# Kernel optimization log

Measured on AMD Instinct MI355X. Metric: run time of the kernel, lower is better.

## Reference

```python
import jax, jax.numpy as jnp
import numpy as np

IN_DIM, HID_DIM, OUT_DIM = 1024, 2048, 1024
DEG1, DEG2 = 8, 8
BATCH = 16384


def cheby_kan_layer(x, coeffs):
    """x: [b, i]; coeffs: [i, o, d+1] -> [b, o].
    Per-feature min-max normalize over batch to [-1,1], Chebyshev recurrence, contract."""
    degree = coeffs.shape[-1] - 1
    mn = jnp.min(x, axis=0, keepdims=True)
    mx = jnp.max(x, axis=0, keepdims=True)
    x = 2.0 * (x - mn) / (mx - mn) - 1.0
    Ts = [jnp.ones_like(x)]
    if degree > 0:
        Ts.append(x)
    for _ in range(2, degree + 1):
        Ts.append(2.0 * x * Ts[-1] - Ts[-2])
    cheby = jnp.stack(Ts, axis=-1)  # [b, i, d+1]
    return jnp.einsum('bid,iod->bo', cheby, coeffs)


def setup_inputs() -> dict:
    key = jax.random.key(0)
    k1, k2, k3 = jax.random.split(key, 3)
    x = jax.random.normal(k1, (BATCH, IN_DIM), dtype=jnp.float32)
    # kaiming-uniform-ish init for coeffs
    b1 = float(np.sqrt(6.0 / IN_DIM))
    b2 = float(np.sqrt(6.0 / HID_DIM))
    coeffs1 = jax.random.uniform(k2, (IN_DIM, HID_DIM, DEG1 + 1), dtype=jnp.float32, minval=-b1, maxval=b1)
    coeffs2 = jax.random.uniform(k3, (HID_DIM, OUT_DIM, DEG2 + 1), dtype=jnp.float32, minval=-b2, maxval=b2)
    return {"x": x, "coeffs1": coeffs1, "coeffs2": coeffs2}


def reference(x, coeffs1, coeffs2):
    h = cheby_kan_layer(x, coeffs1)
    y = cheby_kan_layer(h, coeffs2)
    return y
```

## Files before the change

### kernel.cpp

```cpp
#include <hip/hip_runtime.h>
#include <hip/hip_bf16.h>
#include <stdint.h>


constexpr int BATCH   = 16384;
constexpr int IN_DIM  = 1024;
constexpr int HID_DIM = 2048;
constexpr int OUT_DIM = 1024;
#define DP1 9

using bf16_t = __hip_bfloat16;

typedef __attribute__((ext_vector_type(4))) float f32x4;
typedef __attribute__((ext_vector_type(8))) short s16x8;
typedef __attribute__((ext_vector_type(8))) float f32x8;
typedef __attribute__((ext_vector_type(8))) __bf16 bf16x8;

static __device__ __forceinline__ unsigned int f2bf_u(float f) {
  union { __hip_bfloat16 h; unsigned short u; } cv;
  cv.h = __float2bfloat16(f);
  return (unsigned int)cv.u;
}

template <typename T>
__global__ void kan_minmax_partial(const T* __restrict__ x, int rows, int cols,
                                   float* __restrict__ mnp, float* __restrict__ mxp) {
  const int c  = blockIdx.x * 64 + (threadIdx.x & 63);
  const int rg = threadIdx.x >> 6;
  const int P  = gridDim.y;
  const int chunk = rows / P;
  const int r0 = blockIdx.y * chunk;
  float mn = 1e30f, mx = -1e30f;
  for (int r = r0 + rg; r < r0 + chunk; r += 4) {
    float v = (float)x[(size_t)r * cols + c];
    mn = fminf(mn, v); mx = fmaxf(mx, v);
  }
  __shared__ float smn[256], smx[256];
  smn[threadIdx.x] = mn; smx[threadIdx.x] = mx;
  __syncthreads();
  if (rg == 0) {
    int t = threadIdx.x;
    mn = fminf(fminf(smn[t], smn[t + 64]), fminf(smn[t + 128], smn[t + 192]));
    mx = fmaxf(fmaxf(smx[t], smx[t + 64]), fmaxf(smx[t + 128], smx[t + 192]));
    mnp[(size_t)blockIdx.y * cols + c] = mn;
    mxp[(size_t)blockIdx.y * cols + c] = mx;
  }
}

__global__ void kan_minmax_finalize(const float* __restrict__ mnp, const float* __restrict__ mxp,
                                    int cols, int P, float* __restrict__ s, float* __restrict__ t) {
  int c = blockIdx.x * blockDim.x + threadIdx.x;
  if (c >= cols) return;
  float mn = 1e30f, mx = -1e30f;
  for (int p = 0; p < P; ++p) {
    mn = fminf(mn, mnp[(size_t)p * cols + c]);
    mx = fmaxf(mx, mxp[(size_t)p * cols + c]);
  }
  float inv = 2.0f / (mx - mn);
  s[c] = inv;
  t[c] = -mn * inv - 1.0f;
}

__global__ void kan_repack(const float* __restrict__ coeffs, int I, int O,
                           bf16_t* __restrict__ Bp, float* __restrict__ biasp) {
  const int NIB = I / 32;
  const int ib = blockIdx.x % NIB;
  const int ntile = blockIdx.x / NIB;
  const size_t slab0 = (size_t)(ntile * NIB + ib) * 8 * 8192;
  __shared__ float sb[1024];
  for (int c = threadIdx.x; c < 1024; c += 256) {
    const int l16  = c & 15;
    const int quad = (c >> 4) & 3;
    const int ng   = c >> 6;
    const int o = ntile * 256 + ng * 16 + l16;
    const int ibase = ib * 32 + quad * 8;
    float v[8][9];
#pragma unroll
    for (int q = 0; q < 8; ++q) {
      const float* rp = coeffs + ((size_t)(ibase + q) * O + o) * DP1;
#pragma unroll
      for (int d = 0; d < 9; ++d) v[q][d] = rp[d];
    }
    float bsum = 0.f;
#pragma unroll
    for (int q = 0; q < 8; ++q) bsum += v[q][0];
    sb[c] = bsum;
#pragma unroll
    for (int d = 1; d < 9; ++d) {
      unsigned int pk[4];
#pragma unroll
      for (int q = 0; q < 4; ++q)
        pk[q] = f2bf_u(v[2 * q][d]) | (f2bf_u(v[2 * q + 1][d]) << 16);
      *reinterpret_cast<uint4*>(reinterpret_cast<char*>(Bp) +
          (slab0 + (size_t)(d - 1) * 8192 + (size_t)c * 8) * 2) =
          make_uint4(pk[0], pk[1], pk[2], pk[3]);
    }
  }
  __syncthreads();
  {
    const int t = threadIdx.x;
    const int ng = t >> 4, l16 = t & 15;
    const float s = sb[ng * 64 + l16] + sb[ng * 64 + 16 + l16] +
                    sb[ng * 64 + 32 + l16] + sb[ng * 64 + 48 + l16];
    biasp[(size_t)ib * O + ntile * 256 + t] = s;
  }
}

__global__ void kan_bias_finalize(const float* __restrict__ biasp, int NIB, int O,
                                  float* __restrict__ bias) {
  const int o = blockIdx.x * blockDim.x + threadIdx.x;
  if (o >= O) return;
  float s = 0.f;
  for (int p = 0; p < NIB; ++p) s += biasp[(size_t)p * O + o];
  bias[o] = s;
}

template <typename AT, typename OT>
__launch_bounds__(256, 3)
__global__ void kan_cheby_gemm(const AT* __restrict__ X, const bf16_t* __restrict__ Bp,
                               const float* __restrict__ sc, const float* __restrict__ tc,
                               const float* __restrict__ bias,
                               OT* __restrict__ out, int I, int N) {
  __shared__ __align__(16) short Als[2][2048];
  __shared__ __align__(16) short Bls[2][8192];

  const int m0   = blockIdx.x * 64;
  const int tid  = threadIdx.x;
  const int lane = tid & 63;
  const int wave = tid >> 6;
  const int quad = lane >> 4;
  const int l16  = lane & 15;

  const int ma = tid & 63;
  const int hf = tid >> 6;

  const int NIB = I / 32;
  const int nstage = NIB * 8;
  const size_t slab_base = (size_t)blockIdx.y * NIB * 8 * 8192;

  auto dma_b = [&](int ss) {
    const char* g = reinterpret_cast<const char*>(Bp + slab_base + (size_t)ss * 8192) +
                    wave * 4096 + lane * 16;
    char* l = reinterpret_cast<char*>(&Bls[ss & 1][0]) + wave * 4096;
#pragma unroll
    for (int t = 0; t < 4; ++t)
      __builtin_amdgcn_global_load_lds(
          (const __attribute__((address_space(1))) void*)(g + t * 1024),
          (__attribute__((address_space(3))) void*)(l + t * 1024), 16, 0, 0);
  };

  uint4 rq[2];
  auto load_raw = [&](int ibx) {
    const char* xp = reinterpret_cast<const char*>(
        X + (size_t)(m0 + ma) * I + ibx * 32 + hf * 8);
    if constexpr (sizeof(AT) == 4) {
      rq[0] = *reinterpret_cast<const uint4*>(xp +  0);
      rq[1] = *reinterpret_cast<const uint4*>(xp + 16);
    } else {
      rq[0] = *reinterpret_cast<const uint4*>(xp);
    }
  };

  f32x8 xv, Tm1, Tm2;
#pragma unroll
  for (int j = 0; j < 8; ++j) { xv[j] = 0.f; Tm1[j] = 0.f; Tm2[j] = 0.f; }

  auto unpack_norm = [&](int ibx) {
    const int fbase = ibx * 32 + hf * 8;
    float rv[8];
    const unsigned int* w = reinterpret_cast<const unsigned int*>(rq);
    if constexpr (sizeof(AT) == 4) {
#pragma unroll
      for (int j = 0; j < 8; ++j) rv[j] = __uint_as_float(w[j]);
    } else {
#pragma unroll
      for (int q = 0; q < 4; ++q) {
        rv[2 * q + 0] = __uint_as_float(w[q] << 16);
        rv[2 * q + 1] = __uint_as_float(w[q] & 0xffff0000u);
      }
    }
    const float4* sp = reinterpret_cast<const float4*>(sc + fbase);
    const float4* tp = reinterpret_cast<const float4*>(tc + fbase);
#pragma unroll
    for (int v = 0; v < 2; ++v) {
      float4 s4 = sp[v], t4 = tp[v];
      xv[4 * v + 0] = fmaf(rv[4 * v + 0], s4.x, t4.x);
      xv[4 * v + 1] = fmaf(rv[4 * v + 1], s4.y, t4.y);
      xv[4 * v + 2] = fmaf(rv[4 * v + 2], s4.z, t4.z);
      xv[4 * v + 3] = fmaf(rv[4 * v + 3], s4.w, t4.w);
    }
  };

  auto write_a = [&](int buf, const f32x8& tv) {
    union { bf16x8 v; uint4 q; } u;
    u.v = __builtin_convertvector(tv, bf16x8);
    char* b = reinterpret_cast<char*>(&Als[buf][0]) +
              (ma >> 4) * 1024 + hf * 256 + (ma & 15) * 16;
    *reinterpret_cast<uint4*>(b) = u.q;
  };

  f32x4 acc[4][4] = {};

  load_raw(0);
  dma_b(0);
  unpack_norm(0);
  write_a(0, xv);
  Tm1 = xv;
#pragma unroll
  for (int j = 0; j < 8; ++j) Tm2[j] = 1.0f;
  if (NIB > 1) load_raw(1);
  __syncthreads();

  for (int s = 0; s < nstage; ++s) {
    if (s + 1 < nstage) dma_b(s + 1);

    const char* Ab = reinterpret_cast<const char*>(&Als[s & 1][0]) + lane * 16;
    const char* Bb = reinterpret_cast<const char*>(&Bls[s & 1][0]) + lane * 16;
    s16x8 fa[4], fb[4];
#pragma unroll
    for (int mt = 0; mt < 4; ++mt)
      fa[mt] = *reinterpret_cast<const s16x8*>(Ab + mt * 1024);
#pragma unroll
    for (int nt = 0; nt < 4; ++nt)
      fb[nt] = *reinterpret_cast<const s16x8*>(Bb + (wave * 4 + nt) * 1024);

    if (s + 1 < nstage) {
      const int t = s + 1;
      f32x8 tv;
      if ((t & 7) == 0) {
        const int ibn = t >> 3;
        unpack_norm(ibn);
        if (ibn + 1 < NIB) load_raw(ibn + 1);
        tv = Tm1 = xv;
#pragma unroll
        for (int j = 0; j < 8; ++j) Tm2[j] = 1.0f;
      } else {
        tv = 2.0f * xv * Tm1 - Tm2;
        Tm2 = Tm1; Tm1 = tv;
      }
      write_a(t & 1, tv);
    }

#pragma unroll
    for (int mt = 0; mt < 4; ++mt)
#pragma unroll
      for (int nt = 0; nt < 4; ++nt)
        acc[mt][nt] = __builtin_amdgcn_mfma_f32_16x16x32_bf16(
            fa[mt], fb[nt], acc[mt][nt], 0, 0, 0);

    __syncthreads();
  }

  const int n0 = blockIdx.y * 256;
  float bv[4];
#pragma unroll
  for (int nt = 0; nt < 4; ++nt)
    bv[nt] = bias[n0 + wave * 64 + nt * 16 + l16];
#pragma unroll
  for (int mt = 0; mt < 4; ++mt) {
#pragma unroll
    for (int nt = 0; nt < 4; ++nt) {
      const int n = n0 + wave * 64 + nt * 16 + l16;
#pragma unroll
      for (int r = 0; r < 4; ++r) {
        const int m = m0 + mt * 16 + quad * 4 + r;
        float v = acc[mt][nt][r] + bv[nt];
        if constexpr (sizeof(OT) == 4)
          out[(size_t)m * N + n] = v;
        else
          out[(size_t)m * N + n] = __float2bfloat16(v);
      }
    }
  }
}

extern "C" void kernel_launch(void* const* d_in, const int* in_sizes, int n_in,
                              void* d_out, int out_size, void* d_ws, size_t ws_size,
                              hipStream_t stream) {
  const float* x  = (const float*)d_in[0];
  const float* c1 = (const float*)d_in[1];
  const float* c2 = (const float*)d_in[2];
  float* out = (float*)d_out;

  char* ws = (char*)d_ws;
  size_t off = 0;
  auto take = [&](size_t n) -> char* {
    char* p = ws + off;
    off += (n + 255) & ~(size_t)255;
    return p;
  };
  bf16_t* Bp1 = (bf16_t*)take((size_t)HID_DIM * IN_DIM  * 8 * 2);
  bf16_t* Bp2 = (bf16_t*)take((size_t)OUT_DIM * HID_DIM * 8 * 2);
  bf16_t* h   = (bf16_t*)take((size_t)BATCH * HID_DIM * 2);
  float* s1  = (float*)take(IN_DIM  * 4);
  float* t1  = (float*)take(IN_DIM  * 4);
  float* s2  = (float*)take(HID_DIM * 4);
  float* t2  = (float*)take(HID_DIM * 4);
  float* b1  = (float*)take(HID_DIM * 4);
  float* b2  = (float*)take(OUT_DIM * 4);
  float* bp1 = (float*)take((size_t)(IN_DIM / 32)  * HID_DIM * 4);
  float* bp2 = (float*)take((size_t)(HID_DIM / 32) * OUT_DIM * 4);
  float* mnp = (float*)take((size_t)16 * HID_DIM * 4);
  float* mxp = (float*)take((size_t)16 * HID_DIM * 4);

  kan_minmax_partial<float><<<dim3(IN_DIM / 64, 16), 256, 0, stream>>>(x, BATCH, IN_DIM, mnp, mxp);
  kan_minmax_finalize<<<dim3(IN_DIM / 256), 256, 0, stream>>>(mnp, mxp, IN_DIM, 16, s1, t1);
  kan_repack<<<dim3((HID_DIM / 256) * (IN_DIM / 32)), 256, 0, stream>>>(c1, IN_DIM, HID_DIM, Bp1, bp1);
  kan_bias_finalize<<<dim3(HID_DIM / 256), 256, 0, stream>>>(bp1, IN_DIM / 32, HID_DIM, b1);
  kan_repack<<<dim3((OUT_DIM / 256) * (HID_DIM / 32)), 256, 0, stream>>>(c2, HID_DIM, OUT_DIM, Bp2, bp2);
  kan_bias_finalize<<<dim3(OUT_DIM / 256), 256, 0, stream>>>(bp2, HID_DIM / 32, OUT_DIM, b2);
  kan_cheby_gemm<float, bf16_t><<<dim3(BATCH / 64, HID_DIM / 256), 256, 0, stream>>>(
      x, Bp1, s1, t1, b1, h, IN_DIM, HID_DIM);

  kan_minmax_partial<bf16_t><<<dim3(HID_DIM / 64, 16), 256, 0, stream>>>(h, BATCH, HID_DIM, mnp, mxp);
  kan_minmax_finalize<<<dim3(HID_DIM / 256), 256, 0, stream>>>(mnp, mxp, HID_DIM, 16, s2, t2);
  kan_cheby_gemm<bf16_t, float><<<dim3(BATCH / 64, OUT_DIM / 256), 256, 0, stream>>>(
      h, Bp2, s2, t2, b2, out, HID_DIM, OUT_DIM);
}
```

Baseline: 2.001 ms.

## Split Chebyshev expansion into separate pass and use plain 128x128 tiled GEMM

Unfuses the Chebyshev basis computation from the GEMM. A separate expand kernel writes a pre-tiled bf16 A matrix to workspace in row chunks sized to fit the workspace, and a simpler GEMM with 128x128 block tiles loads both A and B by direct global-to-LDS DMA. The larger tile is meant to halve operand reloads and remove ALU work and register pressure from the MFMA loop. In exchange it adds a large extra round-trip of expanded activations through global memory and more kernel launches.

```diff
diff --git a/kernel.cpp b/kernel.cpp
--- a/kernel.cpp
+++ b/kernel.cpp
@@ -62,184 +62,142 @@
 }
 
 __global__ void kan_repack(const float* __restrict__ coeffs, int I, int O,
-                           bf16_t* __restrict__ Bp, float* __restrict__ biasp) {
-  const int NIB = I / 32;
-  const int ib = blockIdx.x % NIB;
-  const int ntile = blockIdx.x / NIB;
-  const size_t slab0 = (size_t)(ntile * NIB + ib) * 8 * 8192;
-  __shared__ float sb[1024];
-  for (int c = threadIdx.x; c < 1024; c += 256) {
-    const int l16  = c & 15;
-    const int quad = (c >> 4) & 3;
-    const int ng   = c >> 6;
-    const int o = ntile * 256 + ng * 16 + l16;
-    const int ibase = ib * 32 + quad * 8;
-    float v[8][9];
-#pragma unroll
-    for (int q = 0; q < 8; ++q) {
-      const float* rp = coeffs + ((size_t)(ibase + q) * O + o) * DP1;
-#pragma unroll
-      for (int d = 0; d < 9; ++d) v[q][d] = rp[d];
-    }
-    float bsum = 0.f;
-#pragma unroll
-    for (int q = 0; q < 8; ++q) bsum += v[q][0];
-    sb[c] = bsum;
-#pragma unroll
-    for (int d = 1; d < 9; ++d) {
-      unsigned int pk[4];
-#pragma unroll
-      for (int q = 0; q < 4; ++q)
-        pk[q] = f2bf_u(v[2 * q][d]) | (f2bf_u(v[2 * q + 1][d]) << 16);
-      *reinterpret_cast<uint4*>(reinterpret_cast<char*>(Bp) +
-          (slab0 + (size_t)(d - 1) * 8192 + (size_t)c * 8) * 2) =
-          make_uint4(pk[0], pk[1], pk[2], pk[3]);
-    }
+                           bf16_t* __restrict__ Bt, float* __restrict__ biasp) {
+  const int Ktiles = I / 4;
+  const int kt = blockIdx.x % Ktiles;
+  const int nt = blockIdx.x / Ktiles;
+  __shared__ float sb[512];
+  char* tile = reinterpret_cast<char*>(Bt) + ((size_t)nt * Ktiles + kt) * 8192;
+#pragma unroll
+  for (int pp = 0; pp < 2; ++pp) {
+    const int p  = pp * 256 + threadIdx.x;
+    const int ol = p & 127;
+    const int fl = p >> 7;
+    const float* rp = coeffs + ((size_t)(kt * 4 + fl) * O + nt * 128 + ol) * DP1;
+    float v[9];
+#pragma unroll
+    for (int d = 0; d < 9; ++d) v[d] = rp[d];
+    sb[p] = v[0];
+    unsigned int pk[4];
+#pragma unroll
+    for (int q = 0; q < 4; ++q)
+      pk[q] = f2bf_u(v[2 * q + 1]) | (f2bf_u(v[2 * q + 2]) << 16);
+    *reinterpret_cast<uint4*>(tile + (ol >> 4) * 1024 + fl * 256 + (ol & 15) * 16) =
+        make_uint4(pk[0], pk[1], pk[2], pk[3]);
   }
   __syncthreads();
-  {
-    const int t = threadIdx.x;
-    const int ng = t >> 4, l16 = t & 15;
-    const float s = sb[ng * 64 + l16] + sb[ng * 64 + 16 + l16] +
-                    sb[ng * 64 + 32 + l16] + sb[ng * 64 + 48 + l16];
-    biasp[(size_t)ib * O + ntile * 256 + t] = s;
-  }
-}
-
-__global__ void kan_bias_finalize(const float* __restrict__ biasp, int NIB, int O,
+  if (threadIdx.x < 128) {
+    const int ol = threadIdx.x;
+    biasp[(size_t)kt * O + nt * 128 + ol] =
+        sb[ol] + sb[ol + 128] + sb[ol + 256] + sb[ol + 384];
+  }
+}
+
+__global__ void kan_bias_finalize(const float* __restrict__ biasp, int Ktiles, int O,
                                   float* __restrict__ bias) {
   const int o = blockIdx.x * blockDim.x + threadIdx.x;
   if (o >= O) return;
   float s = 0.f;
-  for (int p = 0; p < NIB; ++p) s += biasp[(size_t)p * O + o];
+  for (int p = 0; p < Ktiles; ++p) s += biasp[(size_t)p * O + o];
   bias[o] = s;
 }
 
-template <typename AT, typename OT>
+template <typename AT>
+__global__ void kan_expand(const AT* __restrict__ X, const float* __restrict__ sc,
+                           const float* __restrict__ tc, bf16_t* __restrict__ At,
+                           int I, int r0) {
+  const int Ktiles = I / 4;
+  const int rl = blockIdx.x * 256 + threadIdx.x;
+  const int kt = blockIdx.y;
+  const int f0 = kt * 4;
+  float xv[4];
+  if constexpr (sizeof(AT) == 4) {
+    float4 v = *reinterpret_cast<const float4*>(X + (size_t)(r0 + rl) * I + f0);
+    xv[0] = v.x; xv[1] = v.y; xv[2] = v.z; xv[3] = v.w;
+  } else {
+    uint2 v = *reinterpret_cast<const uint2*>(
+        reinterpret_cast<const char*>(X) + ((size_t)(r0 + rl) * I + f0) * 2);
+    xv[0] = __uint_as_float(v.x << 16);
+    xv[1] = __uint_as_float(v.x & 0xffff0000u);
+    xv[2] = __uint_as_float(v.y << 16);
+    xv[3] = __uint_as_float(v.y & 0xffff0000u);
+  }
+  char* tile = reinterpret_cast<char*>(At) +
+               ((size_t)(rl >> 7) * Ktiles + kt) * 8192 +
+               ((rl & 127) >> 4) * 1024 + (rl & 15) * 16;
+#pragma unroll
+  for (int q = 0; q < 4; ++q) {
+    const float xh = fmaf(xv[q], sc[f0 + q], tc[f0 + q]);
+    f32x8 T;
+    float tm2 = 1.0f, tm1 = xh;
+    T[0] = xh;
+#pragma unroll
+    for (int d = 1; d < 8; ++d) {
+      float t = 2.0f * xh * tm1 - tm2;
+      tm2 = tm1; tm1 = t;
+      T[d] = t;
+    }
+    union { bf16x8 v; uint4 u; } cv;
+    cv.v = __builtin_convertvector(T, bf16x8);
+    *reinterpret_cast<uint4*>(tile + q * 256) = cv.u;
+  }
+}
+
+template <typename OT>
 __launch_bounds__(256, 3)
-__global__ void kan_cheby_gemm(const AT* __restrict__ X, const bf16_t* __restrict__ Bp,
-                               const float* __restrict__ sc, const float* __restrict__ tc,
-                               const float* __restrict__ bias,
-                               OT* __restrict__ out, int I, int N) {
-  __shared__ __align__(16) short Als[2][2048];
-  __shared__ __align__(16) short Bls[2][8192];
-
-  const int m0   = blockIdx.x * 64;
+__global__ void kan_gemm(const bf16_t* __restrict__ At, const bf16_t* __restrict__ Bt,
+                         const float* __restrict__ bias, OT* __restrict__ out,
+                         int Ktiles, int N, int m_off) {
+  __shared__ __align__(16) short Als[2][4096];
+  __shared__ __align__(16) short Bls[2][4096];
+
   const int tid  = threadIdx.x;
   const int lane = tid & 63;
   const int wave = tid >> 6;
+  const int wr   = wave >> 1;
+  const int wc   = wave & 1;
   const int quad = lane >> 4;
   const int l16  = lane & 15;
 
-  const int ma = tid & 63;
-  const int hf = tid >> 6;
-
-  const int NIB = I / 32;
-  const int nstage = NIB * 8;
-  const size_t slab_base = (size_t)blockIdx.y * NIB * 8 * 8192;
-
-  auto dma_b = [&](int ss) {
-    const char* g = reinterpret_cast<const char*>(Bp + slab_base + (size_t)ss * 8192) +
-                    wave * 4096 + lane * 16;
-    char* l = reinterpret_cast<char*>(&Bls[ss & 1][0]) + wave * 4096;
-#pragma unroll
-    for (int t = 0; t < 4; ++t)
+  const char* ga0 = reinterpret_cast<const char*>(At) +
+                    (size_t)blockIdx.x * Ktiles * 8192 + wave * 1024 + lane * 16;
+  const char* gb0 = reinterpret_cast<const char*>(Bt) +
+                    (size_t)blockIdx.y * Ktiles * 8192 + wave * 1024 + lane * 16;
+
+  auto dma = [&](int s) {
+    const int b = s & 1;
+    const char* ga = ga0 + (size_t)s * 8192;
+    const char* gb = gb0 + (size_t)s * 8192;
+    char* la = reinterpret_cast<char*>(&Als[b][0]) + wave * 1024;
+    char* lb = reinterpret_cast<char*>(&Bls[b][0]) + wave * 1024;
+#pragma unroll
+    for (int t = 0; t < 2; ++t) {
       __builtin_amdgcn_global_load_lds(
-          (const __attribute__((address_space(1))) void*)(g + t * 1024),
-          (__attribute__((address_space(3))) void*)(l + t * 1024), 16, 0, 0);
-  };
-
-  uint4 rq[2];
-  auto load_raw = [&](int ibx) {
-    const char* xp = reinterpret_cast<const char*>(
-        X + (size_t)(m0 + ma) * I + ibx * 32 + hf * 8);
-    if constexpr (sizeof(AT) == 4) {
-      rq[0] = *reinterpret_cast<const uint4*>(xp +  0);
-      rq[1] = *reinterpret_cast<const uint4*>(xp + 16);
-    } else {
-      rq[0] = *reinterpret_cast<const uint4*>(xp);
+          (const __attribute__((address_space(1))) void*)(ga + t * 4096),
+          (__attribute__((address_space(3))) void*)(la + t * 4096), 16, 0, 0);
+      __builtin_amdgcn_global_load_lds(
+          (const __attribute__((address_space(1))) void*)(gb + t * 4096),
+          (__attribute__((address_space(3))) void*)(lb + t * 4096), 16, 0, 0);
     }
   };
 
-  f32x8 xv, Tm1, Tm2;
-#pragma unroll
-  for (int j = 0; j < 8; ++j) { xv[j] = 0.f; Tm1[j] = 0.f; Tm2[j] = 0.f; }
-
-  auto unpack_norm = [&](int ibx) {
-    const int fbase = ibx * 32 + hf * 8;
-    float rv[8];
-    const unsigned int* w = reinterpret_cast<const unsigned int*>(rq);
-    if constexpr (sizeof(AT) == 4) {
-#pragma unroll
-      for (int j = 0; j < 8; ++j) rv[j] = __uint_as_float(w[j]);
-    } else {
-#pragma unroll
-      for (int q = 0; q < 4; ++q) {
-        rv[2 * q + 0] = __uint_as_float(w[q] << 16);
-        rv[2 * q + 1] = __uint_as_float(w[q] & 0xffff0000u);
-      }
-    }
-    const float4* sp = reinterpret_cast<const float4*>(sc + fbase);
-    const float4* tp = reinterpret_cast<const float4*>(tc + fbase);
-#pragma unroll
-    for (int v = 0; v < 2; ++v) {
-      float4 s4 = sp[v], t4 = tp[v];
-      xv[4 * v + 0] = fmaf(rv[4 * v + 0], s4.x, t4.x);
-      xv[4 * v + 1] = fmaf(rv[4 * v + 1], s4.y, t4.y);
-      xv[4 * v + 2] = fmaf(rv[4 * v + 2], s4.z, t4.z);
-      xv[4 * v + 3] = fmaf(rv[4 * v + 3], s4.w, t4.w);
-    }
-  };
-
-  auto write_a = [&](int buf, const f32x8& tv) {
-    union { bf16x8 v; uint4 q; } u;
-    u.v = __builtin_convertvector(tv, bf16x8);
-    char* b = reinterpret_cast<char*>(&Als[buf][0]) +
-              (ma >> 4) * 1024 + hf * 256 + (ma & 15) * 16;
-    *reinterpret_cast<uint4*>(b) = u.q;
-  };
-
   f32x4 acc[4][4] = {};
 
-  load_raw(0);
-  dma_b(0);
-  unpack_norm(0);
-  write_a(0, xv);
-  Tm1 = xv;
-#pragma unroll
-  for (int j = 0; j < 8; ++j) Tm2[j] = 1.0f;
-  if (NIB > 1) load_raw(1);
+  dma(0);
   __syncthreads();
 
-  for (int s = 0; s < nstage; ++s) {
-    if (s + 1 < nstage) dma_b(s + 1);
+  for (int s = 0; s < Ktiles; ++s) {
+    if (s + 1 < Ktiles) dma(s + 1);
 
     const char* Ab = reinterpret_cast<const char*>(&Als[s & 1][0]) + lane * 16;
     const char* Bb = reinterpret_cast<const char*>(&Bls[s & 1][0]) + lane * 16;
     s16x8 fa[4], fb[4];
 #pragma unroll
     for (int mt = 0; mt < 4; ++mt)
-      fa[mt] = *reinterpret_cast<const s16x8*>(Ab + mt * 1024);
+      fa[mt] = *reinterpret_cast<const s16x8*>(Ab + (wr * 4 + mt) * 1024);
 #pragma unroll
     for (int nt = 0; nt < 4; ++nt)
-      fb[nt] = *reinterpret_cast<const s16x8*>(Bb + (wave * 4 + nt) * 1024);
-
-    if (s + 1 < nstage) {
-      const int t = s + 1;
-      f32x8 tv;
-      if ((t & 7) == 0) {
-        const int ibn = t >> 3;
-        unpack_norm(ibn);
-        if (ibn + 1 < NIB) load_raw(ibn + 1);
-        tv = Tm1 = xv;
-#pragma unroll
-        for (int j = 0; j < 8; ++j) Tm2[j] = 1.0f;
-      } else {
-        tv = 2.0f * xv * Tm1 - Tm2;
-        Tm2 = Tm1; Tm1 = tv;
-      }
-      write_a(t & 1, tv);
-    }
+      fb[nt] = *reinterpret_cast<const s16x8*>(Bb + (wc * 4 + nt) * 1024);
 
 #pragma unroll
     for (int mt = 0; mt < 4; ++mt)
@@ -251,16 +209,16 @@
     __syncthreads();
   }
 
-  const int n0 = blockIdx.y * 256;
+  const int n0 = blockIdx.y * 128 + wc * 64;
+  const int m0 = m_off + blockIdx.x * 128 + wr * 64;
   float bv[4];
 #pragma unroll
-  for (int nt = 0; nt < 4; ++nt)
-    bv[nt] = bias[n0 + wave * 64 + nt * 16 + l16];
+  for (int nt = 0; nt < 4; ++nt) bv[nt] = bias[n0 + nt * 16 + l16];
 #pragma unroll
   for (int mt = 0; mt < 4; ++mt) {
 #pragma unroll
     for (int nt = 0; nt < 4; ++nt) {
-      const int n = n0 + wave * 64 + nt * 16 + l16;
+      const int n = n0 + nt * 16 + l16;
 #pragma unroll
       for (int r = 0; r < 4; ++r) {
         const int m = m0 + mt * 16 + quad * 4 + r;
@@ -289,8 +247,11 @@
     off += (n + 255) & ~(size_t)255;
     return p;
   };
-  bf16_t* Bp1 = (bf16_t*)take((size_t)HID_DIM * IN_DIM  * 8 * 2);
-  bf16_t* Bp2 = (bf16_t*)take((size_t)OUT_DIM * HID_DIM * 8 * 2);
+  const int KT1 = IN_DIM / 4;
+  const int KT2 = HID_DIM / 4;
+
+  bf16_t* Bt1 = (bf16_t*)take((size_t)(HID_DIM / 128) * KT1 * 8192);
+  bf16_t* Bt2 = (bf16_t*)take((size_t)(OUT_DIM / 128) * KT2 * 8192);
   bf16_t* h   = (bf16_t*)take((size_t)BATCH * HID_DIM * 2);
   float* s1  = (float*)take(IN_DIM  * 4);
   float* t1  = (float*)take(IN_DIM  * 4);
@@ -298,22 +259,37 @@
   float* t2  = (float*)take(HID_DIM * 4);
   float* b1  = (float*)take(HID_DIM * 4);
   float* b2  = (float*)take(OUT_DIM * 4);
-  float* bp1 = (float*)take((size_t)(IN_DIM / 32)  * HID_DIM * 4);
-  float* bp2 = (float*)take((size_t)(HID_DIM / 32) * OUT_DIM * 4);
+  float* bp1 = (float*)take((size_t)KT1 * HID_DIM * 4);
+  float* bp2 = (float*)take((size_t)KT2 * OUT_DIM * 4);
   float* mnp = (float*)take((size_t)16 * HID_DIM * 4);
   float* mxp = (float*)take((size_t)16 * HID_DIM * 4);
 
+  size_t fixed = off;
+  int cm = 1024;
+  for (int c : {8192, 4096, 2048}) {
+    if (fixed + (size_t)c * 16384 * 2 <= ws_size) { cm = c; break; }
+  }
+  bf16_t* A = (bf16_t*)take((size_t)cm * 16384 * 2);
+
   kan_minmax_partial<float><<<dim3(IN_DIM / 64, 16), 256, 0, stream>>>(x, BATCH, IN_DIM, mnp, mxp);
   kan_minmax_finalize<<<dim3(IN_DIM / 256), 256, 0, stream>>>(mnp, mxp, IN_DIM, 16, s1, t1);
-  kan_repack<<<dim3((HID_DIM / 256) * (IN_DIM / 32)), 256, 0, stream>>>(c1, IN_DIM, HID_DIM, Bp1, bp1);
-  kan_bias_finalize<<<dim3(HID_DIM / 256), 256, 0, stream>>>(bp1, IN_DIM / 32, HID_DIM, b1);
-  kan_repack<<<dim3((OUT_DIM / 256) * (HID_DIM / 32)), 256, 0, stream>>>(c2, HID_DIM, OUT_DIM, Bp2, bp2);
-  kan_bias_finalize<<<dim3(OUT_DIM / 256), 256, 0, stream>>>(bp2, HID_DIM / 32, OUT_DIM, b2);
-  kan_cheby_gemm<float, bf16_t><<<dim3(BATCH / 64, HID_DIM / 256), 256, 0, stream>>>(
-      x, Bp1, s1, t1, b1, h, IN_DIM, HID_DIM);
+  kan_repack<<<dim3((HID_DIM / 128) * KT1), 256, 0, stream>>>(c1, IN_DIM, HID_DIM, Bt1, bp1);
+  kan_bias_finalize<<<dim3(HID_DIM / 256), 256, 0, stream>>>(bp1, KT1, HID_DIM, b1);
+  kan_repack<<<dim3((OUT_DIM / 128) * KT2), 256, 0, stream>>>(c2, HID_DIM, OUT_DIM, Bt2, bp2);
+  kan_bias_finalize<<<dim3(OUT_DIM / 256), 256, 0, stream>>>(bp2, KT2, OUT_DIM, b2);
+
+  for (int r0 = 0; r0 < BATCH; r0 += cm) {
+    kan_expand<float><<<dim3(cm / 256, KT1), 256, 0, stream>>>(x, s1, t1, A, IN_DIM, r0);
+    kan_gemm<bf16_t><<<dim3(cm / 128, HID_DIM / 128), 256, 0, stream>>>(
+        A, Bt1, b1, h, KT1, HID_DIM, r0);
+  }
 
   kan_minmax_partial<bf16_t><<<dim3(HID_DIM / 64, 16), 256, 0, stream>>>(h, BATCH, HID_DIM, mnp, mxp);
   kan_minmax_finalize<<<dim3(HID_DIM / 256), 256, 0, stream>>>(mnp, mxp, HID_DIM, 16, s2, t2);
-  kan_cheby_gemm<bf16_t, float><<<dim3(BATCH / 64, OUT_DIM / 256), 256, 0, stream>>>(
-      h, Bp2, s2, t2, b2, out, HID_DIM, OUT_DIM);
-}
+
+  for (int r0 = 0; r0 < BATCH; r0 += cm) {
+    kan_expand<bf16_t><<<dim3(cm / 256, KT2), 256, 0, stream>>>(h, s2, t2, A, HID_DIM, r0);
+    kan_gemm<float><<<dim3(cm / 128, OUT_DIM / 128), 256, 0, stream>>>(
+        A, Bt2, b2, out, KT2, OUT_DIM, r0);
+  }
+}
```

After: 3.017 ms. +50.8%, slower.
